# Kernel tuning notes

Measured on AMD Instinct MI355X. Metric: run time of the kernel, lower is better.

Reference implementation:

```python
import jax, jax.numpy as jnp
import numpy as np

B, R, C, E = 4, 32, 512, 512
H = 8
D = E // H  # 64
EPS = 1e-6


def setup_inputs() -> dict:
    key = jax.random.key(0)
    ks = jax.random.split(key, 9)
    s = 1.0 / np.sqrt(E)  # keep activations in a sane range
    return {
        "x": jax.random.normal(ks[0], (B, R, C, E), jnp.float32),
        "Wq": jax.random.normal(ks[1], (E, E), jnp.float32) * s,
        "bq": jax.random.normal(ks[2], (E,), jnp.float32) * 0.01,
        "Wk": jax.random.normal(ks[3], (E, E), jnp.float32) * s,
        "bk": jax.random.normal(ks[4], (E,), jnp.float32) * 0.01,
        "Wv": jax.random.normal(ks[5], (E, E), jnp.float32) * s,
        "bv": jax.random.normal(ks[6], (E,), jnp.float32) * 0.01,
        "Wo": jax.random.normal(ks[7], (E, E), jnp.float32) * s,
        "bo": jax.random.normal(ks[8], (E,), jnp.float32) * 0.01,
    }


def reference(x, Wq, bq, Wk, bk, Wv, bv, Wo, bo):
    b, r, c, e = x.shape
    # projections (torch Linear: y = x @ W.T + b), split heads -> [b,r,c,H,D]
    q = (x @ Wq.T + bq).reshape(b, r, c, H, D)
    k = (x @ Wk.T + bk).reshape(b, r, c, H, D)
    v = (x @ Wv.T + bv).reshape(b, r, c, H, D)
    # ELU+1 feature map (Performer/linear attention)
    q = jax.nn.elu(q) + 1.0
    k = jax.nn.elu(k) + 1.0
    # K^T V accumulation over the column axis: [b,r,H,D,D]
    ktv = jnp.einsum('brchd,brche->brhde', k, v)
    # normalizer: q . sum_c(k)  -> [b,r,c,H]
    ksum = k.sum(axis=2)  # [b,r,H,D]
    z = 1.0 / (jnp.einsum('brchd,brhd->brch', q, ksum) + EPS)
    # O(N) attention output: [b,r,c,H,D]
    out_h = jnp.einsum('brchd,brhde->brche', q, ktv) * z[..., None]
    out = out_h.reshape(b, r, c, e)
    return out @ Wo.T + bo
```

## Files before the change

### kernel.cpp

```cpp
#include <hip/hip_runtime.h>

typedef unsigned short u16;
typedef short short8 __attribute__((ext_vector_type(8)));
typedef float f32x4 __attribute__((ext_vector_type(4)));

__device__ __forceinline__ u16 f2b(float f) {
  unsigned u = __float_as_uint(f);
  u = u + 0x7FFFu + ((u >> 16) & 1u);
  return (u16)(u >> 16);
}
__device__ __forceinline__ float b2f(u16 b) {
  return __uint_as_float(((unsigned)b) << 16);
}

#define ASYNC_LD16(g, l)                                                                   \
  __builtin_amdgcn_global_load_lds((const __attribute__((address_space(1))) void*)(g),     \
                                   (__attribute__((address_space(3))) void*)(l), 16, 0, 0)

__global__ void convert_x(const float* __restrict__ x, u16* __restrict__ xb) {
  size_t i = ((size_t)blockIdx.x * 256 + threadIdx.x) * 4;
  float4 f = *(const float4*)(x + i);
  ushort4 o;
  o.x = f2b(f.x); o.y = f2b(f.y); o.z = f2b(f.z); o.w = f2b(f.w);
  *(ushort4*)(xb + i) = o;
}

__global__ void convert_w(const float* __restrict__ Wq, const float* __restrict__ Wk,
                          const float* __restrict__ Wv, const float* __restrict__ Wo,
                          u16* __restrict__ Wqkv, u16* __restrict__ Wob) {
  int idx = (blockIdx.x * 256 + threadIdx.x) * 4;
  int row = idx >> 9;
  int col = idx & 511;
  const float* src = (row < 512)    ? Wq + (size_t)row * 512
                     : (row < 1024) ? Wk + (size_t)(row - 512) * 512
                     : (row < 1536) ? Wv + (size_t)(row - 1024) * 512
                                    : Wo + (size_t)(row - 1536) * 512;
  u16* dst = (row < 1536) ? Wqkv + (size_t)row * 512 : Wob + (size_t)(row - 1536) * 512;
  float4 f = *(const float4*)(src + col);
  ushort4 o;
  o.x = f2b(f.x); o.y = f2b(f.y); o.z = f2b(f.z); o.w = f2b(f.w);
  *(ushort4*)(dst + col) = o;
}

__global__ void gemm_qkv(const u16* __restrict__ xb, const u16* __restrict__ Wqkv,
                         const float* __restrict__ bq, const float* __restrict__ bk,
                         const float* __restrict__ bv, u16* __restrict__ Qb,
                         u16* __restrict__ Ktg, u16* __restrict__ Vtg) {
  __shared__ u16 As[128 * 32];
  __shared__ u16 Bs[128 * 32];
  const int tid = threadIdx.x;
  const int blockM = blockIdx.y * 128;
  const int blockN = blockIdx.x * 128;
  const int lane = tid & 63;
  const int w = tid >> 6;
  const int wm = (w & 1) * 64;
  const int wn = (w >> 1) * 64;
  const int lr = lane & 15;
  const int qd = lane >> 4;

  f32x4 acc[4][4];
#pragma unroll
  for (int i = 0; i < 4; ++i)
#pragma unroll
    for (int j = 0; j < 4; ++j) acc[i][j] = {0.f, 0.f, 0.f, 0.f};

  for (int k0 = 0; k0 < 512; k0 += 32) {
    __syncthreads();
#pragma unroll
    for (int j = 0; j < 2; ++j) {
      int idx = j * 256 + tid;
      int row = idx >> 2, seg = idx & 3;
      ASYNC_LD16(xb + (size_t)(blockM + row) * 512 + k0 + seg * 8, As + idx * 8);
      ASYNC_LD16(Wqkv + (size_t)(blockN + row) * 512 + k0 + seg * 8, Bs + idx * 8);
    }
    __syncthreads();
    short8 a[4], b[4];
#pragma unroll
    for (int i = 0; i < 4; ++i) a[i] = *(const short8*)&As[(wm + i * 16 + lr) * 32 + qd * 8];
#pragma unroll
    for (int j = 0; j < 4; ++j) b[j] = *(const short8*)&Bs[(wn + j * 16 + lr) * 32 + qd * 8];
#pragma unroll
    for (int i = 0; i < 4; ++i)
#pragma unroll
      for (int j = 0; j < 4; ++j)
        acc[i][j] = __builtin_amdgcn_mfma_f32_16x16x32_bf16(a[i], b[j], acc[i][j], 0, 0, 0);
  }

  const int which = blockN >> 9;
  const float* bias = which == 0 ? bq : (which == 1 ? bk : bv);
  const int cb = blockN & 511;

  if (which == 0) {
#pragma unroll
    for (int j = 0; j < 4; ++j) {
      int col = cb + wn + j * 16 + lr;
      float bsv = bias[col];
#pragma unroll
      for (int i = 0; i < 4; ++i) {
#pragma unroll
        for (int r = 0; r < 4; ++r) {
          int row = blockM + wm + i * 16 + qd * 4 + r;
          float v = acc[i][j][r] + bsv;
          v = (v > 0.f) ? v + 1.f : __expf(v);
          Qb[(size_t)row * 512 + col] = f2b(v);
        }
      }
    }
  } else {
    u16* dstT = (which == 1) ? Ktg : Vtg;
    const int br = blockM >> 9;
    const int cb0 = (blockM & 511) + wm;
#pragma unroll
    for (int j = 0; j < 4; ++j) {
      int col = cb + wn + j * 16 + lr;
      float bsv = bias[col];
      size_t rowbase = (size_t)br * 262144 + (size_t)col * 512;
#pragma unroll
      for (int i = 0; i < 4; ++i) {
        int c0 = cb0 + i * 16 + qd * 4;
        ushort4 p;
        float v0 = acc[i][j][0] + bsv, v1 = acc[i][j][1] + bsv;
        float v2 = acc[i][j][2] + bsv, v3 = acc[i][j][3] + bsv;
        if (which == 1) {
          v0 = (v0 > 0.f) ? v0 + 1.f : __expf(v0);
          v1 = (v1 > 0.f) ? v1 + 1.f : __expf(v1);
          v2 = (v2 > 0.f) ? v2 + 1.f : __expf(v2);
          v3 = (v3 > 0.f) ? v3 + 1.f : __expf(v3);
        }
        p.x = f2b(v0); p.y = f2b(v1); p.z = f2b(v2); p.w = f2b(v3);
        *(ushort4*)&dstT[rowbase + c0] = p;
      }
    }
  }
}

__global__ void attn(const u16* __restrict__ Qb, const u16* __restrict__ Ktg,
                     const u16* __restrict__ Vtg, u16* __restrict__ Hb) {
  __shared__ u16 KtS[64 * 32];
  __shared__ u16 VtS[64 * 32];
  __shared__ u16 QS[2 * 128 * 32];
  __shared__ u16 ktvT[2 * 64 * 32];
  __shared__ float part[256];
  __shared__ float ksumf[64];
  __shared__ float zs[128];

  const int tid = threadIdx.x;
  const int br = blockIdx.x >> 3;
  const int h = blockIdx.x & 7;
  const int h64 = h * 64;
  const size_t tok0 = (size_t)br * 512;
  const size_t tbase = (size_t)br * 262144 + (size_t)h64 * 512;

  const int lane = tid & 63;
  const int w = tid >> 6;
  const int lr = lane & 15;
  const int qd = lane >> 4;

  const int sc_chan = tid >> 2, sc_seg = tid & 3;

  f32x4 acc[4];
#pragma unroll
  for (int j = 0; j < 4; ++j) acc[j] = {0.f, 0.f, 0.f, 0.f};
  float ks = 0.f;

  for (int ct = 0; ct < 16; ++ct) {
    __syncthreads();
    {
      size_t g = tbase + (size_t)sc_chan * 512 + ct * 32 + sc_seg * 8;
      ASYNC_LD16(Ktg + g, KtS + tid * 8);
      ASYNC_LD16(Vtg + g, VtS + tid * 8);
    }
    __syncthreads();
    short8 a = *(const short8*)&KtS[(w * 16 + lr) * 32 + qd * 8];
#pragma unroll
    for (int j = 0; j < 4; ++j) {
      short8 b = *(const short8*)&VtS[(j * 16 + lr) * 32 + qd * 8];
      acc[j] = __builtin_amdgcn_mfma_f32_16x16x32_bf16(a, b, acc[j], 0, 0, 0);
    }
    ushort4 k0 = *(const ushort4*)&KtS[sc_chan * 32 + sc_seg * 8];
    ushort4 k1 = *(const ushort4*)&KtS[sc_chan * 32 + sc_seg * 8 + 4];
    ks += b2f(k0.x) + b2f(k0.y) + b2f(k0.z) + b2f(k0.w)
        + b2f(k1.x) + b2f(k1.y) + b2f(k1.z) + b2f(k1.w);
  }
  part[tid] = ks;
  {
    int kc = w >> 1;
    int dp = (w & 1) * 16 + qd * 4;
#pragma unroll
    for (int j = 0; j < 4; ++j) {
      int e = j * 16 + lr;
      ushort4 p;
      p.x = f2b(acc[j][0]); p.y = f2b(acc[j][1]);
      p.z = f2b(acc[j][2]); p.w = f2b(acc[j][3]);
      *(ushort4*)&ktvT[kc * 2048 + e * 32 + dp] = p;
    }
  }
  __syncthreads();
  if (tid < 64)
    ksumf[tid] = part[tid * 4] + part[tid * 4 + 1] + part[tid * 4 + 2] + part[tid * 4 + 3];
  __syncthreads();

  short8 bfr[4][2];
#pragma unroll
  for (int j = 0; j < 4; ++j)
#pragma unroll
    for (int kc = 0; kc < 2; ++kc)
      bfr[j][kc] = *(const short8*)&ktvT[kc * 2048 + (j * 16 + lr) * 32 + qd * 8];

  for (int ct = 0; ct < 4; ++ct) {
    __syncthreads();
#pragma unroll
    for (int kc = 0; kc < 2; ++kc)
#pragma unroll
      for (int half = 0; half < 2; ++half)
        ASYNC_LD16(Qb + (tok0 + ct * 128 + half * 64 + sc_chan) * 512 + h64 + kc * 32 + sc_seg * 8,
                   QS + kc * 4096 + half * 2048 + tid * 8);
    __syncthreads();
    if (tid < 128) {
      float s = 0.f;
#pragma unroll 8
      for (int i = 0; i < 32; ++i) {
        int ix = (i + tid) & 31;
        s += b2f(QS[tid * 32 + ix]) * ksumf[ix];
        s += b2f(QS[4096 + tid * 32 + ix]) * ksumf[32 + ix];
      }
      zs[tid] = 1.f / (s + 1e-6f);
    }
    __syncthreads();
#pragma unroll
    for (int s = 0; s < 2; ++s) {
      int mrow = (w * 2 + s) * 16 + lr;
      short8 a0 = *(const short8*)&QS[mrow * 32 + qd * 8];
      short8 a1 = *(const short8*)&QS[4096 + mrow * 32 + qd * 8];
      f32x4 o[4];
#pragma unroll
      for (int j = 0; j < 4; ++j) {
        o[j] = {0.f, 0.f, 0.f, 0.f};
        o[j] = __builtin_amdgcn_mfma_f32_16x16x32_bf16(a0, bfr[j][0], o[j], 0, 0, 0);
        o[j] = __builtin_amdgcn_mfma_f32_16x16x32_bf16(a1, bfr[j][1], o[j], 0, 0, 0);
      }
      int tl = (w * 2 + s) * 16 + qd * 4;
      float z0 = zs[tl], z1 = zs[tl + 1], z2 = zs[tl + 2], z3 = zs[tl + 3];
      size_t gb = (tok0 + ct * 128 + tl) * 512 + h64;
#pragma unroll
      for (int j = 0; j < 4; ++j) {
        int e = j * 16 + lr;
        Hb[gb + e] = f2b(o[j][0] * z0);
        Hb[gb + 512 + e] = f2b(o[j][1] * z1);
        Hb[gb + 1024 + e] = f2b(o[j][2] * z2);
        Hb[gb + 1536 + e] = f2b(o[j][3] * z3);
      }
    }
  }
}

__global__ void gemm_out(const u16* __restrict__ Hb, const u16* __restrict__ Wob,
                         const float* __restrict__ bo, float* __restrict__ out) {
  __shared__ u16 As[128 * 32];
  __shared__ u16 Bs[128 * 32];
  const int tid = threadIdx.x;
  const int blockM = blockIdx.y * 128;
  const int blockN = blockIdx.x * 128;
  const int lane = tid & 63;
  const int w = tid >> 6;
  const int wm = (w & 1) * 64;
  const int wn = (w >> 1) * 64;
  const int lr = lane & 15;
  const int qd = lane >> 4;

  f32x4 acc[4][4];
#pragma unroll
  for (int i = 0; i < 4; ++i)
#pragma unroll
    for (int j = 0; j < 4; ++j) acc[i][j] = {0.f, 0.f, 0.f, 0.f};

  for (int k0 = 0; k0 < 512; k0 += 32) {
    __syncthreads();
#pragma unroll
    for (int j = 0; j < 2; ++j) {
      int idx = j * 256 + tid;
      int row = idx >> 2, seg = idx & 3;
      ASYNC_LD16(Hb + (size_t)(blockM + row) * 512 + k0 + seg * 8, As + idx * 8);
      ASYNC_LD16(Wob + (size_t)(blockN + row) * 512 + k0 + seg * 8, Bs + idx * 8);
    }
    __syncthreads();
    short8 a[4], b[4];
#pragma unroll
    for (int i = 0; i < 4; ++i) a[i] = *(const short8*)&As[(wm + i * 16 + lr) * 32 + qd * 8];
#pragma unroll
    for (int j = 0; j < 4; ++j) b[j] = *(const short8*)&Bs[(wn + j * 16 + lr) * 32 + qd * 8];
#pragma unroll
    for (int i = 0; i < 4; ++i)
#pragma unroll
      for (int j = 0; j < 4; ++j)
        acc[i][j] = __builtin_amdgcn_mfma_f32_16x16x32_bf16(a[i], b[j], acc[i][j], 0, 0, 0);
  }

#pragma unroll
  for (int j = 0; j < 4; ++j) {
    int col = blockN + wn + j * 16 + lr;
    float bsv = bo[col];
#pragma unroll
    for (int i = 0; i < 4; ++i) {
#pragma unroll
      for (int r = 0; r < 4; ++r) {
        int row = blockM + wm + i * 16 + qd * 4 + r;
        out[(size_t)row * 512 + col] = acc[i][j][r] + bsv;
      }
    }
  }
}

extern "C" void kernel_launch(void* const* d_in, const int* in_sizes, int n_in,
                              void* d_out, int out_size, void* d_ws, size_t ws_size,
                              hipStream_t stream) {
  const float* x  = (const float*)d_in[0];
  const float* Wq = (const float*)d_in[1];
  const float* bq = (const float*)d_in[2];
  const float* Wk = (const float*)d_in[3];
  const float* bk = (const float*)d_in[4];
  const float* Wv = (const float*)d_in[5];
  const float* bv = (const float*)d_in[6];
  const float* Wo = (const float*)d_in[7];
  const float* bo = (const float*)d_in[8];
  float* out = (float*)d_out;

  char* ws = (char*)d_ws;
  u16* xb   = (u16*)(ws);
  u16* Wqkv = (u16*)(ws + 0x04000000ull);
  u16* Wob  = (u16*)(ws + 0x04200000ull);
  u16* Qb   = (u16*)(ws + 0x04400000ull);
  u16* Ktg  = (u16*)(ws + 0x08400000ull);
  u16* Vtg  = (u16*)(ws + 0x0C400000ull);
  u16* Hb   = xb;

  hipLaunchKernelGGL(convert_x, dim3(32768), dim3(256), 0, stream, x, xb);
  hipLaunchKernelGGL(convert_w, dim3(1024), dim3(256), 0, stream, Wq, Wk, Wv, Wo, Wqkv, Wob);
  hipLaunchKernelGGL(gemm_qkv, dim3(12, 512), dim3(256), 0, stream, xb, Wqkv, bq, bk, bv, Qb, Ktg, Vtg);
  hipLaunchKernelGGL(attn, dim3(1024), dim3(256), 0, stream, Qb, Ktg, Vtg, Hb);
  hipLaunchKernelGGL(gemm_out, dim3(4, 512), dim3(256), 0, stream, Hb, Wob, bo, out);
}
```

Measured before the change: 501.9 us.

## Rewrite GEMMs with 256x256 tiles, triple-buffered async LDS pipeline, swizzle

```diff
diff --git a/kernel.cpp b/kernel.cpp
--- a/kernel.cpp
+++ b/kernel.cpp
@@ -16,6 +16,13 @@
 #define ASYNC_LD16(g, l)                                                                   \
   __builtin_amdgcn_global_load_lds((const __attribute__((address_space(1))) void*)(g),     \
                                    (__attribute__((address_space(3))) void*)(l), 16, 0, 0)
+
+#define BAR()                                  \
+  do {                                         \
+    asm volatile("" ::: "memory");             \
+    __builtin_amdgcn_s_barrier();              \
+    asm volatile("" ::: "memory");             \
+  } while (0)
 
 __global__ void convert_x(const float* __restrict__ x, u16* __restrict__ xb) {
   size_t i = ((size_t)blockIdx.x * 256 + threadIdx.x) * 4;
@@ -42,91 +49,136 @@
   *(ushort4*)(dst + col) = o;
 }
 
-__global__ void gemm_qkv(const u16* __restrict__ xb, const u16* __restrict__ Wqkv,
-                         const float* __restrict__ bq, const float* __restrict__ bk,
-                         const float* __restrict__ bv, u16* __restrict__ Qb,
-                         u16* __restrict__ Ktg, u16* __restrict__ Vtg) {
-  __shared__ u16 As[128 * 32];
-  __shared__ u16 Bs[128 * 32];
+
+#define STAGE_A(buf, kt)                                                 \
+  do {                                                                   \
+    ASYNC_LD16(Asrc0 + (kt) * 32, S + (buf) * 16384 + tid * 8);          \
+    ASYNC_LD16(Asrc1 + (kt) * 32, S + (buf) * 16384 + 4096 + tid * 8);   \
+  } while (0)
+#define STAGE_B(buf, kt)                                                 \
+  do {                                                                   \
+    ASYNC_LD16(Bsrc0 + (kt) * 32, S + (buf) * 16384 + 8192 + tid * 8);   \
+    ASYNC_LD16(Bsrc1 + (kt) * 32, S + (buf) * 16384 + 12288 + tid * 8);  \
+  } while (0)
+
+#define GEMM_MAIN_LOOP()                                                                     \
+  STAGE_A(0, 0); STAGE_B(0, 0);                                                              \
+  STAGE_A(1, 1); STAGE_B(1, 1);                                                              \
+  asm volatile("s_waitcnt vmcnt(4)" ::: "memory");               \
+  BAR();                                                                                     \
+  int cur = 0, nb = 2;                                                                       \
+  for (int t = 0; t < 16; ++t) {                                                             \
+    const u16* Ab = S + cur * 16384;                                                         \
+    short8 bf[4], af[4];                                                                     \
+                     \
+    if (t < 14) STAGE_A(nb, t + 2);                                                          \
+    _Pragma("unroll") for (int j = 0; j < 4; ++j) bf[j] = *(const short8*)&Ab[rbB + j * 512];\
+    _Pragma("unroll") for (int m = 0; m < 4; ++m) af[m] = *(const short8*)&Ab[rbA + m * 512];\
+    BAR();                                                                                   \
+    __builtin_amdgcn_s_setprio(1);                                                           \
+    _Pragma("unroll") for (int m = 0; m < 4; ++m)                                            \
+      _Pragma("unroll") for (int j = 0; j < 4; ++j)                                          \
+        acc[m][j] = __builtin_amdgcn_mfma_f32_16x16x32_bf16(af[m], bf[j], acc[m][j], 0, 0, 0);\
+    __builtin_amdgcn_s_setprio(0);                                                           \
+                               \
+    if (t < 14) STAGE_B(nb, t + 2);                                                          \
+    _Pragma("unroll") for (int m = 0; m < 4; ++m)                                            \
+        af[m] = *(const short8*)&Ab[rbA + (m + 4) * 512];                                    \
+    BAR();                                                                                   \
+    __builtin_amdgcn_s_setprio(1);                                                           \
+    _Pragma("unroll") for (int m = 0; m < 4; ++m)                                            \
+      _Pragma("unroll") for (int j = 0; j < 4; ++j)                                          \
+        acc[m + 4][j] =                                                                      \
+            __builtin_amdgcn_mfma_f32_16x16x32_bf16(af[m], bf[j], acc[m + 4][j], 0, 0, 0);   \
+    __builtin_amdgcn_s_setprio(0);                                                           \
+         \
+    if (t < 14) asm volatile("s_waitcnt vmcnt(4)" ::: "memory");                             \
+    else        asm volatile("s_waitcnt vmcnt(0)" ::: "memory");                             \
+    BAR();                                                                                   \
+    cur = (cur == 2) ? 0 : cur + 1;                                                          \
+    nb  = (nb == 2)  ? 0 : nb + 1;                                                           \
+  }
+
+__global__ __launch_bounds__(512, 2) void gemm_qkv(
+    const u16* __restrict__ xb, const u16* __restrict__ Wqkv,
+    const float* __restrict__ bq, const float* __restrict__ bk,
+    const float* __restrict__ bv, u16* __restrict__ Qb,
+    u16* __restrict__ Ktg, u16* __restrict__ Vtg) {
+  __shared__ u16 S[49152];
   const int tid = threadIdx.x;
-  const int blockM = blockIdx.y * 128;
-  const int blockN = blockIdx.x * 128;
+  const int bid = blockIdx.x;
+  const int wg = (bid & 7) * 192 + (bid >> 3);
+  const int mtile = wg / 6;
+  const int ntile = wg - mtile * 6;
+  const int blockM = mtile << 8;
+  const int blockN = ntile << 8;
+
   const int lane = tid & 63;
   const int w = tid >> 6;
-  const int wm = (w & 1) * 64;
-  const int wn = (w >> 1) * 64;
+  const int wm = (w >> 2) << 7;
+  const int wn = (w & 3) << 6;
   const int lr = lane & 15;
   const int qd = lane >> 4;
 
-  f32x4 acc[4][4];
-#pragma unroll
-  for (int i = 0; i < 4; ++i)
-#pragma unroll
-    for (int j = 0; j < 4; ++j) acc[i][j] = {0.f, 0.f, 0.f, 0.f};
-
-  for (int k0 = 0; k0 < 512; k0 += 32) {
-    __syncthreads();
-#pragma unroll
-    for (int j = 0; j < 2; ++j) {
-      int idx = j * 256 + tid;
-      int row = idx >> 2, seg = idx & 3;
-      ASYNC_LD16(xb + (size_t)(blockM + row) * 512 + k0 + seg * 8, As + idx * 8);
-      ASYNC_LD16(Wqkv + (size_t)(blockN + row) * 512 + k0 + seg * 8, Bs + idx * 8);
-    }
-    __syncthreads();
-    short8 a[4], b[4];
-#pragma unroll
-    for (int i = 0; i < 4; ++i) a[i] = *(const short8*)&As[(wm + i * 16 + lr) * 32 + qd * 8];
-#pragma unroll
-    for (int j = 0; j < 4; ++j) b[j] = *(const short8*)&Bs[(wn + j * 16 + lr) * 32 + qd * 8];
-#pragma unroll
-    for (int i = 0; i < 4; ++i)
-#pragma unroll
-      for (int j = 0; j < 4; ++j)
-        acc[i][j] = __builtin_amdgcn_mfma_f32_16x16x32_bf16(a[i], b[j], acc[i][j], 0, 0, 0);
-  }
+  const int srow = tid >> 2;
+  const int sg = (tid & 3) ^ (srow & 3);
+  const u16* Asrc0 = xb + (size_t)(blockM + srow) * 512 + sg * 8;
+  const u16* Asrc1 = Asrc0 + 128 * 512;
+  const u16* Bsrc0 = Wqkv + (size_t)(blockN + srow) * 512 + sg * 8;
+  const u16* Bsrc1 = Bsrc0 + 128 * 512;
+
+  const int gsw = (qd ^ (lr & 3)) * 8;
+  const int rbA = (wm + lr) * 32 + gsw;
+  const int rbB = 8192 + (wn + lr) * 32 + gsw;
+
+  f32x4 acc[8][4];
+#pragma unroll
+  for (int m = 0; m < 8; ++m)
+#pragma unroll
+    for (int j = 0; j < 4; ++j) acc[m][j] = {0.f, 0.f, 0.f, 0.f};
+
+  GEMM_MAIN_LOOP();
 
   const int which = blockN >> 9;
-  const float* bias = which == 0 ? bq : (which == 1 ? bk : bv);
   const int cb = blockN & 511;
-
   if (which == 0) {
 #pragma unroll
     for (int j = 0; j < 4; ++j) {
       int col = cb + wn + j * 16 + lr;
-      float bsv = bias[col];
-#pragma unroll
-      for (int i = 0; i < 4; ++i) {
+      float bsv = bq[col];
+#pragma unroll
+      for (int m = 0; m < 8; ++m) {
+        int row = blockM + wm + m * 16 + qd * 4;
 #pragma unroll
         for (int r = 0; r < 4; ++r) {
-          int row = blockM + wm + i * 16 + qd * 4 + r;
-          float v = acc[i][j][r] + bsv;
+          float v = acc[m][j][r] + bsv;
           v = (v > 0.f) ? v + 1.f : __expf(v);
-          Qb[(size_t)row * 512 + col] = f2b(v);
+          Qb[(size_t)(row + r) * 512 + col] = f2b(v);
         }
       }
     }
   } else {
     u16* dstT = (which == 1) ? Ktg : Vtg;
+    const float* bias = (which == 1) ? bk : bv;
     const int br = blockM >> 9;
-    const int cb0 = (blockM & 511) + wm;
+    const int t0 = (blockM & 511) + wm;
 #pragma unroll
     for (int j = 0; j < 4; ++j) {
       int col = cb + wn + j * 16 + lr;
       float bsv = bias[col];
       size_t rowbase = (size_t)br * 262144 + (size_t)col * 512;
 #pragma unroll
-      for (int i = 0; i < 4; ++i) {
-        int c0 = cb0 + i * 16 + qd * 4;
-        ushort4 p;
-        float v0 = acc[i][j][0] + bsv, v1 = acc[i][j][1] + bsv;
-        float v2 = acc[i][j][2] + bsv, v3 = acc[i][j][3] + bsv;
+      for (int m = 0; m < 8; ++m) {
+        int c0 = t0 + m * 16 + qd * 4;
+        float v0 = acc[m][j][0] + bsv, v1 = acc[m][j][1] + bsv;
+        float v2 = acc[m][j][2] + bsv, v3 = acc[m][j][3] + bsv;
         if (which == 1) {
           v0 = (v0 > 0.f) ? v0 + 1.f : __expf(v0);
           v1 = (v1 > 0.f) ? v1 + 1.f : __expf(v1);
           v2 = (v2 > 0.f) ? v2 + 1.f : __expf(v2);
           v3 = (v3 > 0.f) ? v3 + 1.f : __expf(v3);
         }
+        ushort4 p;
         p.x = f2b(v0); p.y = f2b(v1); p.z = f2b(v2); p.w = f2b(v3);
         *(ushort4*)&dstT[rowbase + c0] = p;
       }
@@ -254,59 +306,54 @@
   }
 }
 
-__global__ void gemm_out(const u16* __restrict__ Hb, const u16* __restrict__ Wob,
-                         const float* __restrict__ bo, float* __restrict__ out) {
-  __shared__ u16 As[128 * 32];
-  __shared__ u16 Bs[128 * 32];
+__global__ __launch_bounds__(512, 2) void gemm_out(
+    const u16* __restrict__ Hb, const u16* __restrict__ Wob,
+    const float* __restrict__ bo, float* __restrict__ out) {
+  __shared__ u16 S[49152];
   const int tid = threadIdx.x;
-  const int blockM = blockIdx.y * 128;
-  const int blockN = blockIdx.x * 128;
+  const int bid = blockIdx.x;
+  const int wg = (bid & 7) * 64 + (bid >> 3);
+  const int mtile = wg >> 1;
+  const int ntile = wg & 1;
+  const int blockM = mtile << 8;
+  const int blockN = ntile << 8;
+
   const int lane = tid & 63;
   const int w = tid >> 6;
-  const int wm = (w & 1) * 64;
-  const int wn = (w >> 1) * 64;
+  const int wm = (w >> 2) << 7;
+  const int wn = (w & 3) << 6;
   const int lr = lane & 15;
   const int qd = lane >> 4;
 
-  f32x4 acc[4][4];
-#pragma unroll
-  for (int i = 0; i < 4; ++i)
-#pragma unroll
-    for (int j = 0; j < 4; ++j) acc[i][j] = {0.f, 0.f, 0.f, 0.f};
-
-  for (int k0 = 0; k0 < 512; k0 += 32) {
-    __syncthreads();
-#pragma unroll
-    for (int j = 0; j < 2; ++j) {
-      int idx = j * 256 + tid;
-      int row = idx >> 2, seg = idx & 3;
-      ASYNC_LD16(Hb + (size_t)(blockM + row) * 512 + k0 + seg * 8, As + idx * 8);
-      ASYNC_LD16(Wob + (size_t)(blockN + row) * 512 + k0 + seg * 8, Bs + idx * 8);
-    }
-    __syncthreads();
-    short8 a[4], b[4];
-#pragma unroll
-    for (int i = 0; i < 4; ++i) a[i] = *(const short8*)&As[(wm + i * 16 + lr) * 32 + qd * 8];
-#pragma unroll
-    for (int j = 0; j < 4; ++j) b[j] = *(const short8*)&Bs[(wn + j * 16 + lr) * 32 + qd * 8];
-#pragma unroll
-    for (int i = 0; i < 4; ++i)
-#pragma unroll
-      for (int j = 0; j < 4; ++j)
-        acc[i][j] = __builtin_amdgcn_mfma_f32_16x16x32_bf16(a[i], b[j], acc[i][j], 0, 0, 0);
-  }
+  const int srow = tid >> 2;
+  const int sg = (tid & 3) ^ (srow & 3);
+  const u16* Asrc0 = Hb + (size_t)(blockM + srow) * 512 + sg * 8;
+  const u16* Asrc1 = Asrc0 + 128 * 512;
+  const u16* Bsrc0 = Wob + (size_t)(blockN + srow) * 512 + sg * 8;
+  const u16* Bsrc1 = Bsrc0 + 128 * 512;
+
+  const int gsw = (qd ^ (lr & 3)) * 8;
+  const int rbA = (wm + lr) * 32 + gsw;
+  const int rbB = 8192 + (wn + lr) * 32 + gsw;
+
+  f32x4 acc[8][4];
+#pragma unroll
+  for (int m = 0; m < 8; ++m)
+#pragma unroll
+    for (int j = 0; j < 4; ++j) acc[m][j] = {0.f, 0.f, 0.f, 0.f};
+
+  GEMM_MAIN_LOOP();
 
 #pragma unroll
   for (int j = 0; j < 4; ++j) {
     int col = blockN + wn + j * 16 + lr;
     float bsv = bo[col];
 #pragma unroll
-    for (int i = 0; i < 4; ++i) {
-#pragma unroll
-      for (int r = 0; r < 4; ++r) {
-        int row = blockM + wm + i * 16 + qd * 4 + r;
-        out[(size_t)row * 512 + col] = acc[i][j][r] + bsv;
-      }
+    for (int m = 0; m < 8; ++m) {
+      int row = blockM + wm + m * 16 + qd * 4;
+#pragma unroll
+      for (int r = 0; r < 4; ++r)
+        out[(size_t)(row + r) * 512 + col] = acc[m][j][r] + bsv;
     }
   }
 }
@@ -336,7 +383,7 @@
 
   hipLaunchKernelGGL(convert_x, dim3(32768), dim3(256), 0, stream, x, xb);
   hipLaunchKernelGGL(convert_w, dim3(1024), dim3(256), 0, stream, Wq, Wk, Wv, Wo, Wqkv, Wob);
-  hipLaunchKernelGGL(gemm_qkv, dim3(12, 512), dim3(256), 0, stream, xb, Wqkv, bq, bk, bv, Qb, Ktg, Vtg);
+  hipLaunchKernelGGL(gemm_qkv, dim3(1536), dim3(512), 0, stream, xb, Wqkv, bq, bk, bv, Qb, Ktg, Vtg);
   hipLaunchKernelGGL(attn, dim3(1024), dim3(256), 0, stream, Qb, Ktg, Vtg, Hb);
-  hipLaunchKernelGGL(gemm_out, dim3(4, 512), dim3(256), 0, stream, Hb, Wob, bo, out);
-}
+  hipLaunchKernelGGL(gemm_out, dim3(512), dim3(512), 0, stream, Hb, Wob, bo, out);
+}
```

After: 476.6 us. 5.0% less time.
